# Optimization experiments

Hardware: AMD Instinct MI355X
Metric: run time of the kernel (lower is better)

## Reference

```python
import jax, jax.numpy as jnp
import numpy as np

BETA = 0.25

def setup_inputs() -> dict:
    key = jax.random.key(0)
    k1, k2 = jax.random.split(key)
    x = jax.random.normal(k1, (32, 32, 32, 64), dtype=jnp.float32)
    # tf.random_uniform_initializer default: uniform in [-0.05, 0.05]
    embeddings = jax.random.uniform(k2, (64, 1024), dtype=jnp.float32,
                                    minval=-0.05, maxval=0.05)
    return {"x": x, "embeddings": embeddings}

def reference(x, embeddings):
    D, K = embeddings.shape
    flat = x.reshape(-1, D)                                   # [N, D]
    # squared L2 distances to each codebook vector (expanded form)
    sim = flat @ embeddings                                   # [N, K]
    dists = (jnp.sum(flat * flat, axis=1, keepdims=True)
             + jnp.sum(embeddings * embeddings, axis=0)
             - 2.0 * sim)                                     # [N, K]
    idx = jnp.argmin(dists, axis=1)                           # [N]
    quantized = embeddings.T[idx].reshape(x.shape)            # gather == one-hot matmul
    commitment_loss = BETA * jnp.mean((jax.lax.stop_gradient(quantized) - x) ** 2)
    codebook_loss = jnp.mean((quantized - jax.lax.stop_gradient(x)) ** 2)
    loss = commitment_loss + codebook_loss
    out = x + jax.lax.stop_gradient(quantized - x)            # straight-through
    return out, loss
```

## Files before the change

### kernel.cpp

```cpp
#include <hip/hip_runtime.h>
#include <hip/hip_bf16.h>


#define NROWS 32768
#define DDIM  64
#define KCODE 1024
#define NELEM (NROWS * DDIM)
#define MARGIN 4e-3f
#define MAINBLK 256

typedef __attribute__((ext_vector_type(8))) _Float16 f16x8;
typedef __attribute__((ext_vector_type(4))) float f32x4;

static __device__ __forceinline__ unsigned short f2h(float v) {
    _Float16 h = (_Float16)v;
    unsigned short b;
    __builtin_memcpy(&b, &h, 2);
    return b;
}
static __device__ __forceinline__ void gload16(const void* g, void* l) {
    __builtin_amdgcn_global_load_lds(
        (const __attribute__((address_space(1))) void*)g,
        (__attribute__((address_space(3))) void*)l, 16, 0, 0);
}

__global__ void vq_prep(const float* __restrict__ e,
                        float* __restrict__ se,
                        float* __restrict__ eT,
                        unsigned short* __restrict__ ehSw,
                        int* __restrict__ ctrl) {
    __shared__ float tile[64][17];
    const int t = threadIdx.x;
    const int k0 = blockIdx.x * 16;
    if (blockIdx.x == 0 && t < 4) ctrl[t] = 0;
    #pragma unroll
    for (int i = 0; i < 4; ++i) {
        int idx = i * 256 + t;
        int d = idx >> 4, kk = idx & 15;
        tile[d][kk] = e[d * KCODE + k0 + kk];
    }
    __syncthreads();
    if (t < 16) {
        float s = 0.f;
        #pragma unroll
        for (int d = 0; d < 64; ++d) { float v = tile[d][t]; s = fmaf(v, v, s); }
        se[k0 + t] = s;
    }
    const int kk = t >> 4;
    const int dg = (t & 15) * 4;
    const int kg = k0 + kk;
    float v0 = tile[dg + 0][kk], v1 = tile[dg + 1][kk];
    float v2 = tile[dg + 2][kk], v3 = tile[dg + 3][kk];
    *(float4*)&eT[(size_t)kg * 64 + dg] = make_float4(v0, v1, v2, v3);
    const int sw = (((dg >> 3) ^ (kg & 7)) << 3) + (dg & 7);
    *(ushort4*)&ehSw[(size_t)kg * 64 + sw] =
        make_ushort4(f2h(v0), f2h(v1), f2h(v2), f2h(v3));
}

__launch_bounds__(512)
__global__ void vq_main(const float* __restrict__ x,
                        const float* __restrict__ se,
                        const float* __restrict__ eT,
                        const unsigned short* __restrict__ ehSw,
                        float* __restrict__ out,
                        float* __restrict__ parts,
                        int* __restrict__ done) {
    __shared__ unsigned short Beh[KCODE * 64];
    __shared__ float sse[KCODE];
    __shared__ float wsum[8];
    __shared__ float xs[64];
    __shared__ float cb[512];
    __shared__ int   ci[512];
    __shared__ int   lightRows[128];
    __shared__ int   lightA[128];
    __shared__ int   lightB[128];
    __shared__ int   heavyRows[128];
    __shared__ int   idxRow[128];
    __shared__ int   sNl, sNh;
    __shared__ int   lastS;

    const int t = threadIdx.x;
    const int lane = t & 63;
    const int w = t >> 6;
    const int quad = lane >> 4, l15 = lane & 15;
    const int rowBase = blockIdx.x * 128 + w * 16;

    if (t == 0) { sNl = 0; sNh = 0; }

    {
        const unsigned char* g = (const unsigned char*)ehSw;
        #pragma unroll
        for (int r = 0; r < 16; ++r)
            gload16(g + (size_t)(r * 512 + t) * 16, &Beh[(r * 512 + t) * 8]);
        float2 s2 = ((const float2*)se)[t];
        sse[2 * t + 0] = s2.x;
        sse[2 * t + 1] = s2.y;
    }

    f16x8 ah0, ah1, al0, al1;
    {
        const float4* ap0 = (const float4*)(x + (size_t)(rowBase + l15) * 64 + quad * 8);
        const float4* ap1 = (const float4*)(x + (size_t)(rowBase + l15) * 64 + 32 + quad * 8);
        float4 a0 = ap0[0], a1 = ap0[1], b0 = ap1[0], b1 = ap1[1];
        float av[8] = {a0.x, a0.y, a0.z, a0.w, a1.x, a1.y, a1.z, a1.w};
        float bv[8] = {b0.x, b0.y, b0.z, b0.w, b1.x, b1.y, b1.z, b1.w};
        f16x8 h0, h1, l0, l1;
        #pragma unroll
        for (int j = 0; j < 8; ++j) {
            _Float16 ha = (_Float16)av[j];
            _Float16 hb = (_Float16)bv[j];
            h0[j] = ha;
            h1[j] = hb;
            l0[j] = (_Float16)(av[j] - (float)ha);
            l1[j] = (_Float16)(bv[j] - (float)hb);
        }
        ah0 = h0; ah1 = h1; al0 = l0; al1 = l1;
    }
    __syncthreads();

    float sb[4], sb2[4], sb3[4];
    int   si[4], si2[4];
    #pragma unroll
    for (int r = 0; r < 4; ++r) {
        sb[r] = 3.4e38f; sb2[r] = 3.4e38f; sb3[r] = 3.4e38f;
        si[r] = 0; si2[r] = 0;
    }

    const int slot0 = ((quad ^ (l15 & 7)) << 3);
    const int slot1 = (((quad + 4) ^ (l15 & 7)) << 3);

    #pragma unroll 4
    for (int nt = 0; nt < 64; ++nt) {
        const int code = nt * 16 + l15;
        f16x8 b0 = *(const f16x8*)&Beh[code * 64 + slot0];
        f16x8 b1 = *(const f16x8*)&Beh[code * 64 + slot1];
        float cse = sse[code];
        f32x4 aA = {0.f, 0.f, 0.f, 0.f}, aB = {0.f, 0.f, 0.f, 0.f};
        aA = __builtin_amdgcn_mfma_f32_16x16x32_f16(ah0, b0, aA, 0, 0, 0);
        aB = __builtin_amdgcn_mfma_f32_16x16x32_f16(ah1, b1, aB, 0, 0, 0);
        aA = __builtin_amdgcn_mfma_f32_16x16x32_f16(al0, b0, aA, 0, 0, 0);
        aB = __builtin_amdgcn_mfma_f32_16x16x32_f16(al1, b1, aB, 0, 0, 0);
        #pragma unroll
        for (int r = 0; r < 4; ++r) {
            float key = fmaf(-2.f, aA[r] + aB[r], cse);
            bool lt1 = key < sb[r];
            bool lt2 = key < sb2[r];
            bool lt3 = key < sb3[r];
            sb3[r] = lt2 ? sb2[r] : (lt3 ? key : sb3[r]);
            float nsb2 = lt1 ? sb[r] : (lt2 ? key : sb2[r]);
            int   nsi2 = lt1 ? si[r] : (lt2 ? code : si2[r]);
            sb[r]  = lt1 ? key  : sb[r];
            si[r]  = lt1 ? code : si[r];
            sb2[r] = nsb2;
            si2[r] = nsi2;
        }
    }

    #pragma unroll
    for (int m = 1; m < 16; m <<= 1) {
        #pragma unroll
        for (int r = 0; r < 4; ++r) {
            float b1 = __shfl_xor(sb[r],  m, 64);
            int   i1 = __shfl_xor(si[r],  m, 64);
            float b2 = __shfl_xor(sb2[r], m, 64);
            int   i2 = __shfl_xor(si2[r], m, 64);
            float b3 = __shfl_xor(sb3[r], m, 64);
            bool t1 = (b1 < sb[r]) || (b1 == sb[r] && i1 < si[r]);
            float w1 = t1 ? b1 : sb[r];    int wi1 = t1 ? i1 : si[r];
            float l1 = t1 ? sb[r] : b1;    int li1 = t1 ? si[r] : i1;
            float c2 = t1 ? b2 : sb2[r];   int ci2 = t1 ? i2 : si2[r];
            float c3 = t1 ? b3 : sb3[r];
            float o2 = t1 ? sb2[r] : b2;
            bool t2 = (c2 < l1) || (c2 == l1 && ci2 < li1);
            float w2 = t2 ? c2 : l1;       int wi2 = t2 ? ci2 : li1;
            float w3 = t2 ? fminf(l1, c3) : fminf(c2, o2);
            sb[r] = w1; si[r] = wi1; sb2[r] = w2; si2[r] = wi2; sb3[r] = w3;
        }
    }

    if (l15 == 0) {
        #pragma unroll
        for (int r = 0; r < 4; ++r) {
            const int rloc = w * 16 + quad * 4 + r;
            idxRow[rloc] = si[r];
            if (sb2[r] - sb[r] < MARGIN) {
                if (sb3[r] - sb[r] < MARGIN) {
                    int p = atomicAdd(&sNh, 1);
                    heavyRows[p] = rloc;
                } else {
                    int p = atomicAdd(&sNl, 1);
                    lightRows[p] = rloc;
                    lightA[p] = si[r];
                    lightB[p] = si2[r];
                }
            }
        }
    }
    __syncthreads();

    const int nl = sNl;
    const int nh = sNh;
    if (t < 2 * nl) {
        const int j = t >> 1, s = t & 1;
        const int rloc = lightRows[j];
        const int code = s ? lightB[j] : lightA[j];
        const float4* xr = (const float4*)(x + ((size_t)blockIdx.x * 128 + rloc) * 64);
        const float4* er = (const float4*)(eT + (size_t)code * 64);
        float sx = 0.f, dot = 0.f;
        #pragma unroll
        for (int i4 = 0; i4 < 16; ++i4) {
            float4 xv = xr[i4];
            float4 ev = er[i4];
            sx = fmaf(xv.x, xv.x, sx); sx = fmaf(xv.y, xv.y, sx);
            sx = fmaf(xv.z, xv.z, sx); sx = fmaf(xv.w, xv.w, sx);
            dot = fmaf(xv.x, ev.x, dot); dot = fmaf(xv.y, ev.y, dot);
            dot = fmaf(xv.z, ev.z, dot); dot = fmaf(xv.w, ev.w, dot);
        }
        float dd = (sx + sse[code]) - 2.0f * dot;
        float ddo = __shfl_xor(dd, 1, 64);
        int   ido = __shfl_xor(code, 1, 64);
        bool take = (ddo < dd) || (ddo == dd && ido < code);
        int best = take ? ido : code;
        if (s == 0) idxRow[rloc] = best;
    }

    for (int i = 0; i < nh; ++i) {
        const int rloc = heavyRows[i];
        const size_t grow = (size_t)blockIdx.x * 128 + rloc;
        if (t < 64) xs[t] = x[grow * 64 + t];
        __syncthreads();

        float sx = 0.f;
        #pragma unroll
        for (int d = 0; d < 64; ++d) sx = fmaf(xs[d], xs[d], sx);

        const int k0 = t * 2;
        const float4* e0 = (const float4*)(eT + (size_t)(k0 + 0) * 64);
        const float4* e1 = (const float4*)(eT + (size_t)(k0 + 1) * 64);
        float dot0 = 0.f, dot1 = 0.f;
        #pragma unroll
        for (int i4 = 0; i4 < 16; ++i4) {
            float4 v0 = e0[i4], v1 = e1[i4];
            float xa = xs[4 * i4 + 0], xb = xs[4 * i4 + 1];
            float xc = xs[4 * i4 + 2], xd = xs[4 * i4 + 3];
            dot0 = fmaf(xa, v0.x, dot0); dot0 = fmaf(xb, v0.y, dot0);
            dot0 = fmaf(xc, v0.z, dot0); dot0 = fmaf(xd, v0.w, dot0);
            dot1 = fmaf(xa, v1.x, dot1); dot1 = fmaf(xb, v1.y, dot1);
            dot1 = fmaf(xc, v1.z, dot1); dot1 = fmaf(xd, v1.w, dot1);
        }
        float dd0 = (sx + sse[k0 + 0]) - 2.0f * dot0;
        float dd1 = (sx + sse[k0 + 1]) - 2.0f * dot1;
        float db = dd0; int di = k0;
        if (dd1 < db) { db = dd1; di = k0 + 1; }
        cb[t] = db; ci[t] = di;
        __syncthreads();

        if (t < 64) {
            float B = cb[t]; int I = ci[t];
            #pragma unroll
            for (int s = 64; s < 512; s += 64) {
                float b = cb[t + s]; int i2 = ci[t + s];
                bool take = (b < B) || (b == B && i2 < I);
                B = take ? b : B;
                I = take ? i2 : I;
            }
            #pragma unroll
            for (int m = 1; m < 64; m <<= 1) {
                float ob = __shfl_xor(B, m, 64);
                int   oi = __shfl_xor(I, m, 64);
                bool take = (ob < B) || (ob == B && oi < I);
                B = take ? ob : B;
                I = take ? oi : I;
            }
            if (t == 0) idxRow[rloc] = I;
        }
        __syncthreads();
    }
    __syncthreads();

    const int myidx = idxRow[w * 16 + l15];
    {
        const float4* qrow = (const float4*)(eT + (size_t)myidx * 64 + quad * 16);
        const float4* xrow = (const float4*)(x + (size_t)(rowBase + l15) * 64 + quad * 16);
        float4* orow = (float4*)(out + (size_t)(rowBase + l15) * 64 + quad * 16);
        float lsum = 0.f;
        #pragma unroll
        for (int i = 0; i < 4; ++i) {
            float4 q = qrow[i];
            float4 xv = xrow[i];
            float4 o;
            float dx;
            dx = q.x - xv.x; o.x = xv.x + dx; lsum = fmaf(dx, dx, lsum);
            dx = q.y - xv.y; o.y = xv.y + dx; lsum = fmaf(dx, dx, lsum);
            dx = q.z - xv.z; o.z = xv.z + dx; lsum = fmaf(dx, dx, lsum);
            dx = q.w - xv.w; o.w = xv.w + dx; lsum = fmaf(dx, dx, lsum);
            orow[i] = o;
        }
        #pragma unroll
        for (int off = 32; off > 0; off >>= 1)
            lsum += __shfl_down(lsum, off, 64);
        if (lane == 0) wsum[w] = lsum;
    }
    __syncthreads();

    if (t == 0) {
        float s = 0.f;
        #pragma unroll
        for (int i = 0; i < 8; ++i) s += wsum[i];
        __hip_atomic_store(&parts[blockIdx.x], s, __ATOMIC_RELEASE,
                           __HIP_MEMORY_SCOPE_AGENT);
        int fin = __hip_atomic_fetch_add(done, 1, __ATOMIC_ACQ_REL,
                                         __HIP_MEMORY_SCOPE_AGENT);
        lastS = (fin == MAINBLK - 1) ? 1 : 0;
    }
    __syncthreads();
    if (lastS) {
        if (t < 256)
            cb[t] = __hip_atomic_load(&parts[t], __ATOMIC_ACQUIRE,
                                      __HIP_MEMORY_SCOPE_AGENT);
        __syncthreads();
        if (t < 64) {
            float v = cb[t] + cb[t + 64] + cb[t + 128] + cb[t + 192];
            #pragma unroll
            for (int off = 32; off > 0; off >>= 1)
                v += __shfl_down(v, off, 64);
            if (t == 0) {
                float m = v / (float)NELEM;
                out[NELEM] = 0.25f * m + m;
            }
        }
    }
}

extern "C" void kernel_launch(void* const* d_in, const int* in_sizes, int n_in,
                              void* d_out, int out_size, void* d_ws, size_t ws_size,
                              hipStream_t stream) {
    const float* x = (const float*)d_in[0];
    const float* e = (const float*)d_in[1];
    float* out = (float*)d_out;
    float* ws  = (float*)d_ws;

    int*   done          = (int*)(ws + 2);
    float* se            = ws + 64;
    float* eT            = ws + 1280;
    unsigned short* ehSw = (unsigned short*)(ws + 66816);
    float* parts         = ws + 165120;

    vq_prep<<<64, 256, 0, stream>>>(e, se, eT, ehSw, (int*)ws);
    vq_main<<<MAINBLK, 512, 0, stream>>>(x, se, eT, ehSw, out, parts, done);
}
```

Baseline: 114.2 us.

## Split codebook scan across two wave groups with 1024-thread blocks

Doubles the block to 1024 threads. Each half of the waves scans half of the codebook for the same 128 rows, and the two halves' top-3 candidates are merged through shared memory before the ambiguity classification. The heavy-row brute-force path now gives one code per thread, and only the first 8 waves write outputs and loss. The aim is more resident waves per CU to hide LDS and MFMA latency, since the 128KB LDS codebook allows only one block per CU. The cost is a tighter per-thread register budget under the 1024 launch bound, plus an extra merge pass and barrier.

```diff
diff --git a/kernel.cpp b/kernel.cpp
--- a/kernel.cpp
+++ b/kernel.cpp
@@ -57,7 +57,7 @@
         make_ushort4(f2h(v0), f2h(v1), f2h(v2), f2h(v3));
 }
 
-__launch_bounds__(512)
+__launch_bounds__(1024)
 __global__ void vq_main(const float* __restrict__ x,
                         const float* __restrict__ se,
                         const float* __restrict__ eT,
@@ -69,8 +69,10 @@
     __shared__ float sse[KCODE];
     __shared__ float wsum[8];
     __shared__ float xs[64];
-    __shared__ float cb[512];
-    __shared__ int   ci[512];
+    __shared__ float cb[1024];
+    __shared__ int   ci[1024];
+    __shared__ float hv1[2][128], hv2[2][128], hv3[2][128];
+    __shared__ int   hi1[2][128], hi2[2][128];
     __shared__ int   lightRows[128];
     __shared__ int   lightA[128];
     __shared__ int   lightB[128];
@@ -82,19 +84,19 @@
     const int t = threadIdx.x;
     const int lane = t & 63;
     const int w = t >> 6;
+    const int w8 = w & 7;
+    const int half = w >> 3;
     const int quad = lane >> 4, l15 = lane & 15;
-    const int rowBase = blockIdx.x * 128 + w * 16;
+    const int rowBase = blockIdx.x * 128 + w8 * 16;
 
     if (t == 0) { sNl = 0; sNh = 0; }
 
     {
         const unsigned char* g = (const unsigned char*)ehSw;
         #pragma unroll
-        for (int r = 0; r < 16; ++r)
-            gload16(g + (size_t)(r * 512 + t) * 16, &Beh[(r * 512 + t) * 8]);
-        float2 s2 = ((const float2*)se)[t];
-        sse[2 * t + 0] = s2.x;
-        sse[2 * t + 1] = s2.y;
+        for (int r = 0; r < 8; ++r)
+            gload16(g + (size_t)(r * 1024 + t) * 16, &Beh[(r * 1024 + t) * 8]);
+        sse[t] = se[t];
     }
 
     f16x8 ah0, ah1, al0, al1;
@@ -128,10 +130,11 @@
 
     const int slot0 = ((quad ^ (l15 & 7)) << 3);
     const int slot1 = (((quad + 4) ^ (l15 & 7)) << 3);
+    const int codeBase = half * 512;
 
     #pragma unroll 4
-    for (int nt = 0; nt < 64; ++nt) {
-        const int code = nt * 16 + l15;
+    for (int nt = 0; nt < 32; ++nt) {
+        const int code = codeBase + nt * 16 + l15;
         f16x8 b0 = *(const f16x8*)&Beh[code * 64 + slot0];
         f16x8 b1 = *(const f16x8*)&Beh[code * 64 + slot1];
         float cse = sse[code];
@@ -181,18 +184,41 @@
     if (l15 == 0) {
         #pragma unroll
         for (int r = 0; r < 4; ++r) {
-            const int rloc = w * 16 + quad * 4 + r;
-            idxRow[rloc] = si[r];
-            if (sb2[r] - sb[r] < MARGIN) {
-                if (sb3[r] - sb[r] < MARGIN) {
-                    int p = atomicAdd(&sNh, 1);
-                    heavyRows[p] = rloc;
-                } else {
-                    int p = atomicAdd(&sNl, 1);
-                    lightRows[p] = rloc;
-                    lightA[p] = si[r];
-                    lightB[p] = si2[r];
-                }
+            const int rloc = w8 * 16 + quad * 4 + r;
+            hv1[half][rloc] = sb[r];  hi1[half][rloc] = si[r];
+            hv2[half][rloc] = sb2[r]; hi2[half][rloc] = si2[r];
+            hv3[half][rloc] = sb3[r];
+        }
+    }
+    __syncthreads();
+
+    if (t < 128) {
+        float a1 = hv1[0][t]; int ai1 = hi1[0][t];
+        float a2 = hv2[0][t]; int ai2 = hi2[0][t];
+        float a3 = hv3[0][t];
+        float b1 = hv1[1][t]; int bi1 = hi1[1][t];
+        float b2 = hv2[1][t]; int bi2 = hi2[1][t];
+        float b3 = hv3[1][t];
+        bool t1 = (b1 < a1) || (b1 == a1 && bi1 < ai1);
+        float w1 = t1 ? b1 : a1;   int wi1 = t1 ? bi1 : ai1;
+        float l1 = t1 ? a1 : b1;   int li1 = t1 ? ai1 : bi1;
+        float c2 = t1 ? b2 : a2;   int ci2 = t1 ? bi2 : ai2;
+        float c3 = t1 ? b3 : a3;
+        float o2 = t1 ? a2 : b2;
+        bool t2 = (c2 < l1) || (c2 == l1 && ci2 < li1);
+        float w2 = t2 ? c2 : l1;   int wi2 = t2 ? ci2 : li1;
+        float w3 = t2 ? fminf(l1, c3) : fminf(c2, o2);
+
+        idxRow[t] = wi1;
+        if (w2 - w1 < MARGIN) {
+            if (w3 - w1 < MARGIN) {
+                int p = atomicAdd(&sNh, 1);
+                heavyRows[p] = t;
+            } else {
+                int p = atomicAdd(&sNl, 1);
+                lightRows[p] = t;
+                lightA[p] = wi1;
+                lightB[p] = wi2;
             }
         }
     }
@@ -234,31 +260,24 @@
         #pragma unroll
         for (int d = 0; d < 64; ++d) sx = fmaf(xs[d], xs[d], sx);
 
-        const int k0 = t * 2;
-        const float4* e0 = (const float4*)(eT + (size_t)(k0 + 0) * 64);
-        const float4* e1 = (const float4*)(eT + (size_t)(k0 + 1) * 64);
-        float dot0 = 0.f, dot1 = 0.f;
+        const float4* e0 = (const float4*)(eT + (size_t)t * 64);
+        float dot0 = 0.f;
         #pragma unroll
         for (int i4 = 0; i4 < 16; ++i4) {
-            float4 v0 = e0[i4], v1 = e1[i4];
+            float4 v0 = e0[i4];
             float xa = xs[4 * i4 + 0], xb = xs[4 * i4 + 1];
             float xc = xs[4 * i4 + 2], xd = xs[4 * i4 + 3];
             dot0 = fmaf(xa, v0.x, dot0); dot0 = fmaf(xb, v0.y, dot0);
             dot0 = fmaf(xc, v0.z, dot0); dot0 = fmaf(xd, v0.w, dot0);
-            dot1 = fmaf(xa, v1.x, dot1); dot1 = fmaf(xb, v1.y, dot1);
-            dot1 = fmaf(xc, v1.z, dot1); dot1 = fmaf(xd, v1.w, dot1);
-        }
-        float dd0 = (sx + sse[k0 + 0]) - 2.0f * dot0;
-        float dd1 = (sx + sse[k0 + 1]) - 2.0f * dot1;
-        float db = dd0; int di = k0;
-        if (dd1 < db) { db = dd1; di = k0 + 1; }
-        cb[t] = db; ci[t] = di;
+        }
+        float dd0 = (sx + sse[t]) - 2.0f * dot0;
+        cb[t] = dd0; ci[t] = t;
         __syncthreads();
 
         if (t < 64) {
             float B = cb[t]; int I = ci[t];
             #pragma unroll
-            for (int s = 64; s < 512; s += 64) {
+            for (int s = 64; s < 1024; s += 64) {
                 float b = cb[t + s]; int i2 = ci[t + s];
                 bool take = (b < B) || (b == B && i2 < I);
                 B = take ? b : B;
@@ -278,8 +297,8 @@
     }
     __syncthreads();
 
-    const int myidx = idxRow[w * 16 + l15];
-    {
+    if (w < 8) {
+        const int myidx = idxRow[w * 16 + l15];
         const float4* qrow = (const float4*)(eT + (size_t)myidx * 64 + quad * 16);
         const float4* xrow = (const float4*)(x + (size_t)(rowBase + l15) * 64 + quad * 16);
         float4* orow = (float4*)(out + (size_t)(rowBase + l15) * 64 + quad * 16);
@@ -347,5 +366,5 @@
     float* parts         = ws + 165120;
 
     vq_prep<<<64, 256, 0, stream>>>(e, se, eT, ehSw, (int*)ws);
-    vq_main<<<MAINBLK, 512, 0, stream>>>(x, se, eT, ehSw, out, parts, done);
-}
+    vq_main<<<MAINBLK, 1024, 0, stream>>>(x, se, eT, ehSw, out, parts, done);
+}
```

Measured after the change: 113.2 us. About the same (-0.8%).

## Split codebook across waves, read fp16 codebook from global, 1024 blocks of 32 rows

Applied to the files above, without the earlier changes.

Each block now handles 32 rows instead of 128. Its eight waves split the 1024 codes into four quarters, and each wave reads its fp16 codebook slice straight from global memory/L2 rather than staging the full 128KB codebook in LDS. The per-quarter top-3 results are merged in shared memory by one thread per row before the ambiguous-row refinement. This drops the large LDS footprint and the per-block staging cost so more blocks fit per CU, at the price of uncached-in-LDS codebook reads, an extra merge step, and four times more blocks each doing its own setup and atomic finalisation.

```diff
diff --git a/kernel.cpp b/kernel.cpp
--- a/kernel.cpp
+++ b/kernel.cpp
@@ -7,7 +7,8 @@
 #define KCODE 1024
 #define NELEM (NROWS * DDIM)
 #define MARGIN 4e-3f
-#define MAINBLK 256
+#define GRID_MAIN 1024
+#define TPB 512
 
 typedef __attribute__((ext_vector_type(8))) _Float16 f16x8;
 typedef __attribute__((ext_vector_type(4))) float f32x4;
@@ -18,16 +19,11 @@
     __builtin_memcpy(&b, &h, 2);
     return b;
 }
-static __device__ __forceinline__ void gload16(const void* g, void* l) {
-    __builtin_amdgcn_global_load_lds(
-        (const __attribute__((address_space(1))) void*)g,
-        (__attribute__((address_space(3))) void*)l, 16, 0, 0);
-}
 
 __global__ void vq_prep(const float* __restrict__ e,
                         float* __restrict__ se,
                         float* __restrict__ eT,
-                        unsigned short* __restrict__ ehSw,
+                        unsigned short* __restrict__ ehL,
                         int* __restrict__ ctrl) {
     __shared__ float tile[64][17];
     const int t = threadIdx.x;
@@ -52,46 +48,44 @@
     float v0 = tile[dg + 0][kk], v1 = tile[dg + 1][kk];
     float v2 = tile[dg + 2][kk], v3 = tile[dg + 3][kk];
     *(float4*)&eT[(size_t)kg * 64 + dg] = make_float4(v0, v1, v2, v3);
-    const int sw = (((dg >> 3) ^ (kg & 7)) << 3) + (dg & 7);
-    *(ushort4*)&ehSw[(size_t)kg * 64 + sw] =
+    *(ushort4*)&ehL[(size_t)kg * 64 + dg] =
         make_ushort4(f2h(v0), f2h(v1), f2h(v2), f2h(v3));
 }
 
-__launch_bounds__(512)
+__launch_bounds__(TPB, 6)
 __global__ void vq_main(const float* __restrict__ x,
                         const float* __restrict__ se,
                         const float* __restrict__ eT,
-                        const unsigned short* __restrict__ ehSw,
+                        const unsigned short* __restrict__ ehL,
                         float* __restrict__ out,
                         float* __restrict__ parts,
                         int* __restrict__ done) {
-    __shared__ unsigned short Beh[KCODE * 64];
     __shared__ float sse[KCODE];
-    __shared__ float wsum[8];
+    __shared__ float wsum[2];
     __shared__ float xs[64];
     __shared__ float cb[512];
     __shared__ int   ci[512];
-    __shared__ int   lightRows[128];
-    __shared__ int   lightA[128];
-    __shared__ int   lightB[128];
-    __shared__ int   heavyRows[128];
-    __shared__ int   idxRow[128];
+    __shared__ float hv1[4][32], hv2[4][32], hv3[4][32];
+    __shared__ int   hi1[4][32], hi2[4][32];
+    __shared__ int   lightRows[32];
+    __shared__ int   lightA[32];
+    __shared__ int   lightB[32];
+    __shared__ int   heavyRows[32];
+    __shared__ int   idxRow[32];
     __shared__ int   sNl, sNh;
     __shared__ int   lastS;
 
     const int t = threadIdx.x;
     const int lane = t & 63;
     const int w = t >> 6;
+    const int rowGroup = w & 1;
+    const int quarter = w >> 1;
     const int quad = lane >> 4, l15 = lane & 15;
-    const int rowBase = blockIdx.x * 128 + w * 16;
+    const int rowBase = blockIdx.x * 32 + rowGroup * 16;
 
     if (t == 0) { sNl = 0; sNh = 0; }
 
     {
-        const unsigned char* g = (const unsigned char*)ehSw;
-        #pragma unroll
-        for (int r = 0; r < 16; ++r)
-            gload16(g + (size_t)(r * 512 + t) * 16, &Beh[(r * 512 + t) * 8]);
         float2 s2 = ((const float2*)se)[t];
         sse[2 * t + 0] = s2.x;
         sse[2 * t + 1] = s2.y;
@@ -126,14 +120,14 @@
         si[r] = 0; si2[r] = 0;
     }
 
-    const int slot0 = ((quad ^ (l15 & 7)) << 3);
-    const int slot1 = (((quad + 4) ^ (l15 & 7)) << 3);
+    const int codeBase = quarter * 256;
+    const unsigned short* ehp = ehL + (size_t)(codeBase + l15) * 64 + quad * 8;
 
     #pragma unroll 4
-    for (int nt = 0; nt < 64; ++nt) {
-        const int code = nt * 16 + l15;
-        f16x8 b0 = *(const f16x8*)&Beh[code * 64 + slot0];
-        f16x8 b1 = *(const f16x8*)&Beh[code * 64 + slot1];
+    for (int nt = 0; nt < 16; ++nt) {
+        const int code = codeBase + nt * 16 + l15;
+        f16x8 b0 = *(const f16x8*)(ehp + nt * 1024);
+        f16x8 b1 = *(const f16x8*)(ehp + nt * 1024 + 32);
         float cse = sse[code];
         f32x4 aA = {0.f, 0.f, 0.f, 0.f}, aB = {0.f, 0.f, 0.f, 0.f};
         aA = __builtin_amdgcn_mfma_f32_16x16x32_f16(ah0, b0, aA, 0, 0, 0);
@@ -181,18 +175,56 @@
     if (l15 == 0) {
         #pragma unroll
         for (int r = 0; r < 4; ++r) {
-            const int rloc = w * 16 + quad * 4 + r;
-            idxRow[rloc] = si[r];
-            if (sb2[r] - sb[r] < MARGIN) {
-                if (sb3[r] - sb[r] < MARGIN) {
-                    int p = atomicAdd(&sNh, 1);
-                    heavyRows[p] = rloc;
-                } else {
-                    int p = atomicAdd(&sNl, 1);
-                    lightRows[p] = rloc;
-                    lightA[p] = si[r];
-                    lightB[p] = si2[r];
-                }
+            const int rloc = rowGroup * 16 + quad * 4 + r;
+            hv1[quarter][rloc] = sb[r];  hi1[quarter][rloc] = si[r];
+            hv2[quarter][rloc] = sb2[r]; hi2[quarter][rloc] = si2[r];
+            hv3[quarter][rloc] = sb3[r];
+        }
+    }
+    __syncthreads();
+
+    if (t < 32) {
+        float m1[3], mv2[3], m3[3];
+        int   mi1[3], mi2[3];
+        #pragma unroll
+        for (int s = 0; s < 3; ++s) {
+            float a1, a2, a3, b1, b2, b3;
+            int ai1, ai2, bi1, bi2;
+            if (s < 2) {
+                a1 = hv1[2*s][t];   ai1 = hi1[2*s][t];
+                a2 = hv2[2*s][t];   ai2 = hi2[2*s][t];
+                a3 = hv3[2*s][t];
+                b1 = hv1[2*s+1][t]; bi1 = hi1[2*s+1][t];
+                b2 = hv2[2*s+1][t]; bi2 = hi2[2*s+1][t];
+                b3 = hv3[2*s+1][t];
+            } else {
+                a1 = m1[0]; ai1 = mi1[0]; a2 = mv2[0]; ai2 = mi2[0]; a3 = m3[0];
+                b1 = m1[1]; bi1 = mi1[1]; b2 = mv2[1]; bi2 = mi2[1]; b3 = m3[1];
+            }
+            bool t1 = (b1 < a1) || (b1 == a1 && bi1 < ai1);
+            float w1 = t1 ? b1 : a1;   int wi1 = t1 ? bi1 : ai1;
+            float l1 = t1 ? a1 : b1;   int li1 = t1 ? ai1 : bi1;
+            float c2 = t1 ? b2 : a2;   int ci2 = t1 ? bi2 : ai2;
+            float c3 = t1 ? b3 : a3;
+            float o2 = t1 ? a2 : b2;
+            bool t2 = (c2 < l1) || (c2 == l1 && ci2 < li1);
+            float w2 = t2 ? c2 : l1;   int wi2 = t2 ? ci2 : li1;
+            float w3 = t2 ? fminf(l1, c3) : fminf(c2, o2);
+            m1[s] = w1; mi1[s] = wi1; mv2[s] = w2; mi2[s] = wi2; m3[s] = w3;
+        }
+        const float w1 = m1[2], w2 = mv2[2], w3 = m3[2];
+        const int wi1 = mi1[2], wi2 = mi2[2];
+
+        idxRow[t] = wi1;
+        if (w2 - w1 < MARGIN) {
+            if (w3 - w1 < MARGIN) {
+                int p = atomicAdd(&sNh, 1);
+                heavyRows[p] = t;
+            } else {
+                int p = atomicAdd(&sNl, 1);
+                lightRows[p] = t;
+                lightA[p] = wi1;
+                lightB[p] = wi2;
             }
         }
     }
@@ -204,7 +236,7 @@
         const int j = t >> 1, s = t & 1;
         const int rloc = lightRows[j];
         const int code = s ? lightB[j] : lightA[j];
-        const float4* xr = (const float4*)(x + ((size_t)blockIdx.x * 128 + rloc) * 64);
+        const float4* xr = (const float4*)(x + ((size_t)blockIdx.x * 32 + rloc) * 64);
         const float4* er = (const float4*)(eT + (size_t)code * 64);
         float sx = 0.f, dot = 0.f;
         #pragma unroll
@@ -226,7 +258,7 @@
 
     for (int i = 0; i < nh; ++i) {
         const int rloc = heavyRows[i];
-        const size_t grow = (size_t)blockIdx.x * 128 + rloc;
+        const size_t grow = (size_t)blockIdx.x * 32 + rloc;
         if (t < 64) xs[t] = x[grow * 64 + t];
         __syncthreads();
 
@@ -278,8 +310,8 @@
     }
     __syncthreads();
 
-    const int myidx = idxRow[w * 16 + l15];
-    {
+    if (w < 2) {
+        const int myidx = idxRow[w * 16 + l15];
         const float4* qrow = (const float4*)(eT + (size_t)myidx * 64 + quad * 16);
         const float4* xrow = (const float4*)(x + (size_t)(rowBase + l15) * 64 + quad * 16);
         float4* orow = (float4*)(out + (size_t)(rowBase + l15) * 64 + quad * 16);
@@ -304,23 +336,27 @@
     __syncthreads();
 
     if (t == 0) {
-        float s = 0.f;
-        #pragma unroll
-        for (int i = 0; i < 8; ++i) s += wsum[i];
+        float s = wsum[0] + wsum[1];
         __hip_atomic_store(&parts[blockIdx.x], s, __ATOMIC_RELEASE,
                            __HIP_MEMORY_SCOPE_AGENT);
         int fin = __hip_atomic_fetch_add(done, 1, __ATOMIC_ACQ_REL,
                                          __HIP_MEMORY_SCOPE_AGENT);
-        lastS = (fin == MAINBLK - 1) ? 1 : 0;
+        lastS = (fin == GRID_MAIN - 1) ? 1 : 0;
     }
     __syncthreads();
     if (lastS) {
-        if (t < 256)
-            cb[t] = __hip_atomic_load(&parts[t], __ATOMIC_ACQUIRE,
-                                      __HIP_MEMORY_SCOPE_AGENT);
+        {
+            float pa = __hip_atomic_load(&parts[t], __ATOMIC_ACQUIRE,
+                                         __HIP_MEMORY_SCOPE_AGENT);
+            float pb = __hip_atomic_load(&parts[t + 512], __ATOMIC_ACQUIRE,
+                                         __HIP_MEMORY_SCOPE_AGENT);
+            cb[t] = pa + pb;
+        }
         __syncthreads();
         if (t < 64) {
-            float v = cb[t] + cb[t + 64] + cb[t + 128] + cb[t + 192];
+            float v = cb[t];
+            #pragma unroll
+            for (int s = 64; s < 512; s += 64) v += cb[t + s];
             #pragma unroll
             for (int off = 32; off > 0; off >>= 1)
                 v += __shfl_down(v, off, 64);
@@ -343,9 +379,9 @@
     int*   done          = (int*)(ws + 2);
     float* se            = ws + 64;
     float* eT            = ws + 1280;
-    unsigned short* ehSw = (unsigned short*)(ws + 66816);
+    unsigned short* ehL  = (unsigned short*)(ws + 66816);
     float* parts         = ws + 165120;
 
-    vq_prep<<<64, 256, 0, stream>>>(e, se, eT, ehSw, (int*)ws);
-    vq_main<<<MAINBLK, 512, 0, stream>>>(x, se, eT, ehSw, out, parts, done);
+    vq_prep<<<64, 256, 0, stream>>>(e, se, eT, ehL, (int*)ws);
+    vq_main<<<GRID_MAIN, TPB, 0, stream>>>(x, se, eT, ehL, out, parts, done);
 }
```

Result: slower. 212.0 us (+85.7%).
